# Optimization experiments

Measured on AMD Instinct MI355X. Metric: run time of the kernel, lower is better.

## Reference

```python
import jax, jax.numpy as jnp
import numpy as np

N = 16384      # nodes (radar cells x batched graphs)
H = 128        # n_hidden
N_ENV = 7
N_IN = N_ENV + 2 + 1  # env + coords + density = 10
T_CTX = 24
HORIZON = 40
T = T_CTX + HORIZON


def setup_inputs() -> dict:
    key = jax.random.key(0)
    ks = jax.random.split(key, 40)

    def w(k, shape, fan_in):
        return jax.random.normal(k, shape, jnp.float32) * np.float32(1.0 / np.sqrt(fan_in))

    inp = {}
    inp["x"] = jax.random.normal(ks[0], (N, T), jnp.float32)
    inp["coords"] = jax.random.normal(ks[1], (N, 2), jnp.float32)
    inp["env"] = jax.random.normal(ks[2], (N, N_ENV, T), jnp.float32)
    # --- encoder params ---
    inp["enc_W_in"] = w(ks[3], (H, N_IN), N_IN)           # Linear(n_in->H), no bias
    inp["enc_Wih0"] = w(ks[4], (4 * H, H), H)
    inp["enc_Whh0"] = w(ks[5], (4 * H, H), H)
    inp["enc_bih0"] = jnp.zeros((4 * H,), jnp.float32)
    inp["enc_bhh0"] = jnp.zeros((4 * H,), jnp.float32)
    inp["enc_Wih1"] = w(ks[6], (4 * H, H), H)
    inp["enc_Whh1"] = w(ks[7], (4 * H, H), H)
    inp["enc_bih1"] = jnp.zeros((4 * H,), jnp.float32)
    inp["enc_bhh1"] = jnp.zeros((4 * H,), jnp.float32)
    # --- NodeLSTM params ---
    inp["node_W_in"] = w(ks[8], (H, N_IN), N_IN)          # Linear(n_in->H), no bias
    inp["in_Wih"] = w(ks[9], (4 * H, 2 * H), 2 * H)       # lstm_in takes [inputs, enc_state]
    inp["in_Whh"] = w(ks[10], (4 * H, H), H)
    inp["in_bih"] = jnp.zeros((4 * H,), jnp.float32)
    inp["in_bhh"] = jnp.zeros((4 * H,), jnp.float32)
    inp["l1_Wih"] = w(ks[11], (4 * H, H), H)
    inp["l1_Whh"] = w(ks[12], (4 * H, H), H)
    inp["l1_bih"] = jnp.zeros((4 * H,), jnp.float32)
    inp["l1_bhh"] = jnp.zeros((4 * H,), jnp.float32)
    # hidden2in / hidden2out heads: Linear(H,H) -> ReLU -> Linear(H,1)
    inp["h2in_W1"] = w(ks[13], (H, H), H)
    inp["h2in_b1"] = jnp.zeros((H,), jnp.float32)
    inp["h2in_W2"] = w(ks[14], (1, H), H)
    inp["h2in_b2"] = jnp.zeros((1,), jnp.float32)
    inp["h2out_W1"] = w(ks[15], (H, H), H)
    inp["h2out_b1"] = jnp.zeros((H,), jnp.float32)
    inp["h2out_W2"] = w(ks[16], (1, H), H)
    inp["h2out_b2"] = jnp.zeros((1,), jnp.float32)
    return inp


def _lstm_cell(xin, h, c, Wih, Whh, bih, bhh):
    # torch.nn.LSTMCell semantics; gate order i, f, g, o
    gates = xin @ Wih.T + h @ Whh.T + (bih + bhh)
    i, f, g, o = jnp.split(gates, 4, axis=1)
    c_new = jax.nn.sigmoid(f) * c + jax.nn.sigmoid(i) * jnp.tanh(g)
    h_new = jax.nn.sigmoid(o) * jnp.tanh(c_new)
    return h_new, c_new


def reference(x, coords, env,
              enc_W_in, enc_Wih0, enc_Whh0, enc_bih0, enc_bhh0,
              enc_Wih1, enc_Whh1, enc_bih1, enc_bhh1,
              node_W_in, in_Wih, in_Whh, in_bih, in_bhh,
              l1_Wih, l1_Whh, l1_bih, l1_bhh,
              h2in_W1, h2in_b1, h2in_W2, h2in_b2,
              h2out_W1, h2out_b1, h2out_W2, h2out_b2):
    n = x.shape[0]
    z = jnp.zeros((n, H), x.dtype)

    # ---------- encoder: scan over T_CTX context steps ----------
    def enc_step(carry, xs):
        h0, c0, h1, c1 = carry
        xt, et = xs  # [N], [N, N_ENV]
        inp = jnp.concatenate([xt[:, None], coords, et], axis=1) @ enc_W_in.T
        h0, c0 = _lstm_cell(inp, h0, c0, enc_Wih0, enc_Whh0, enc_bih0, enc_bhh0)
        h1, c1 = _lstm_cell(h0, h1, c1, enc_Wih1, enc_Whh1, enc_bih1, enc_bhh1)
        return (h0, c0, h1, c1), None

    enc_xs = (x[:, :T_CTX].T, jnp.moveaxis(env[:, :, :T_CTX], 2, 0))
    (h0, c0, h1, c1), _ = jax.lax.scan(enc_step, (z, z, z, z), enc_xs)
    enc_state = h1  # h[-1] captured at setup_states, fixed over the horizon

    def head(hid, W1, b1, W2, b2):
        return jax.nn.sigmoid(jax.nn.relu(hid @ W1.T + b1) @ W2.T + b2)

    # ---------- decoder: scan over HORIZON forecast steps ----------
    def dec_step(carry, et):
        xc, h0, c0, h1, c1 = carry
        inp = jnp.concatenate([xc, coords, et], axis=1) @ node_W_in.T
        inp = jnp.concatenate([inp, enc_state], axis=1)  # [N, 2H]
        h0, c0 = _lstm_cell(inp, h0, c0, in_Wih, in_Whh, in_bih, in_bhh)
        h1, c1 = _lstm_cell(h0, h1, c1, l1_Wih, l1_Whh, l1_bih, l1_bhh)
        x_in = head(h1, h2in_W1, h2in_b1, h2in_W2, h2in_b2)
        x_out = head(h1, h2out_W1, h2out_b1, h2out_W2, h2out_b2)
        xn = xc + x_in - x_out * xc  # source/sink update, [N, 1]
        return (xn, h0, c0, h1, c1), xn

    x0 = x[:, T_CTX - 1][:, None]
    dec_xs = jnp.moveaxis(env[:, :, T_CTX:T_CTX + HORIZON], 2, 0)
    _, ys = jax.lax.scan(dec_step, (x0, h0, c0, h1, c1), dec_xs)  # [HORIZON, N, 1]
    return jnp.transpose(ys[..., 0], (1, 0))  # [N, HORIZON]
```

## Files before the change

kernel.cpp:

```cpp
#include <hip/hip_runtime.h>
#include <hip/hip_bf16.h>
#include <cstdint>
#include <cstddef>

typedef __bf16 bf16_t;
typedef bf16_t bf16x8 __attribute__((ext_vector_type(8)));
typedef bf16_t bf16x4 __attribute__((ext_vector_type(4)));
typedef float  f32x4  __attribute__((ext_vector_type(4)));

#define TT    64
#define T_CTX 24
#define HOR   40
#define SA    264
#define NTH   512

#define MFMA __builtin_amdgcn_mfma_f32_16x16x32_bf16

#define O_PKE   16
#define O_PKD   (O_PKE + 262144)
#define O_PKX   (O_PKD + 294912)
#define O_BIAS  (O_PKX + 131072)
#define O_HEADP (O_BIAS + 2048)
#define O_WINE  (O_HEADP + 512)
#define O_WINN  (O_WINE + 1536)
#define O_B2    (O_WINN + 1536)

struct Ptrs { const void* q[29]; };

__device__ __forceinline__ float sigm(float x) {
  return __builtin_amdgcn_rcpf(1.f + __expf(-x));
}
__device__ __forceinline__ float tanh_(float x) {
  return 1.f - 2.f * __builtin_amdgcn_rcpf(1.f + __expf(2.f * x));
}
__device__ __forceinline__ unsigned pk2(float a, float b) {
  unsigned ua = __float_as_uint(a), ub = __float_as_uint(b);
  ua = (ua + 0x7fffu + ((ua >> 16) & 1u)) >> 16;
  ub = (ub + 0x7fffu + ((ub >> 16) & 1u)) >> 16;
  return ua | (ub << 16);
}
__device__ __forceinline__ float uplo(unsigned p){ return __uint_as_float(p << 16); }
__device__ __forceinline__ float uphi(unsigned p){ return __uint_as_float(p & 0xffff0000u); }

__global__ void detect_kernel(const unsigned short* __restrict__ wsrc, int* __restrict__ flag)
{
  int tid = threadIdx.x;
  int wild = 0;
  for (int i = tid; i < 256; i += 64) {
    unsigned short b = wsrc[i];
    float v  = __uint_as_float(((unsigned)b) << 16);
    float av = fabsf(v);
    unsigned e = (b >> 7) & 0xff;
    if (av > 1000.f || e == 0xff || (((b & 0x7fff) != 0) && av < 1e-9f)) wild++;
  }
  for (int off = 32; off; off >>= 1) wild += __shfl_down(wild, off, 64);
  if (tid == 0) flag[0] = (wild > 16) ? 1 : 0;
}

__global__ void prep_kernel(Ptrs P, bf16_t* __restrict__ wb, const int* __restrict__ flag)
{
  const bool f32 = (flag[0] != 0);
  const int gtid = blockIdx.x * blockDim.x + threadIdx.x;
  const int gsz  = gridDim.x * blockDim.x;
  auto rd = [&](const void* src, int i) -> float {
    return f32 ? ((const float*)src)[i] : (float)((const bf16_t*)src)[i];
  };

  for (int i = gtid; i < 262144; i += gsz) {
    int w = i >> 15, r = i & 32767, f = r >> 9, e = r & 511;
    int ln = e >> 3, j = e & 7;
    int seg = f >> 5, fk = f & 31, kt = fk >> 2, g = fk & 3;
    int row = g * 128 + w * 16 + (ln & 15);
    int col = kt * 32 + ((ln >> 4) << 3) + j;
    float v;
    if (seg == 0) v = (col < 128) ? rd(P.q[4], row * 128 + col) : rd(P.q[5], row * 128 + col - 128);
    else          v = (col < 128) ? rd(P.q[8], row * 128 + col) : rd(P.q[9], row * 128 + col - 128);
    wb[O_PKE + i] = (bf16_t)v;
  }
  for (int i = gtid; i < 294912; i += gsz) {
    int w = i / 36864, r = i - w * 36864, f = r >> 9, e = r & 511;
    int ln = e >> 3, j = e & 7;
    int colk = ((ln >> 4) << 3) + j;
    float v;
    if (f < 64) {
      int seg = f >> 5, fk = f & 31, kt = fk >> 2, g = fk & 3;
      int row = g * 128 + w * 16 + (ln & 15);
      int col = kt * 32 + colk;
      if (seg == 0) v = (col < 128) ? rd(P.q[13], row * 256 + col) : rd(P.q[14], row * 128 + col - 128);
      else          v = (col < 128) ? rd(P.q[17], row * 128 + col) : rd(P.q[18], row * 128 + col - 128);
    } else {
      int f2 = f - 64, h = f2 >> 2, kt = f2 & 3;
      int row = w * 16 + (ln & 15);
      int col = kt * 32 + colk;
      v = rd(h ? P.q[25] : P.q[21], row * 128 + col);
    }
    wb[O_PKD + i] = (bf16_t)v;
  }
  for (int i = gtid; i < 131072; i += gsz) {
    int w = i >> 14, r = i & 16383, f = r >> 9, e = r & 511;
    int ln = e >> 3, j = e & 7;
    int kt = f >> 2, g = f & 3;
    int row = g * 128 + w * 16 + (ln & 15);
    int col = kt * 32 + ((ln >> 4) << 3) + j;
    wb[O_PKX + i] = (bf16_t)rd(P.q[13], row * 256 + 128 + col);
  }
  for (int i = gtid; i < 512; i += gsz) {
    wb[O_BIAS + i]        = (bf16_t)(rd(P.q[6],  i) + rd(P.q[7],  i));
    wb[O_BIAS + 512 + i]  = (bf16_t)(rd(P.q[10], i) + rd(P.q[11], i));
    wb[O_BIAS + 1024 + i] = (bf16_t)(rd(P.q[15], i) + rd(P.q[16], i));
    wb[O_BIAS + 1536 + i] = (bf16_t)(rd(P.q[19], i) + rd(P.q[20], i));
  }
  for (int i = gtid; i < 128; i += gsz) {
    wb[O_HEADP + i]       = (bf16_t)rd(P.q[22], i);
    wb[O_HEADP + 128 + i] = (bf16_t)rd(P.q[23], i);
    wb[O_HEADP + 256 + i] = (bf16_t)rd(P.q[26], i);
    wb[O_HEADP + 384 + i] = (bf16_t)rd(P.q[27], i);
  }
  for (int i = gtid; i < 1536; i += gsz) {
    int cc = i / 12, j = i % 12;
    wb[O_WINE + i] = (j < 10) ? (bf16_t)rd(P.q[3],  cc * 10 + j) : (bf16_t)0.f;
    wb[O_WINN + i] = (j < 10) ? (bf16_t)rd(P.q[12], cc * 10 + j) : (bf16_t)0.f;
  }
  if (gtid == 0) {
    wb[O_B2]     = (bf16_t)rd(P.q[24], 0);
    wb[O_B2 + 1] = (bf16_t)rd(P.q[28], 0);
  }
}

struct PreB { bf16x8 b[2][4]; };

__device__ __forceinline__ PreB preB(const bf16_t* __restrict__ pl) {
  PreB r;
#pragma unroll
  for (int p = 0; p < 2; ++p)
#pragma unroll
    for (int g = 0; g < 4; ++g)
      r.b[p][g] = *(const bf16x8*)(pl + (p * 4 + g) * 512);
  return r;
}

template<int NKT>
__device__ __forceinline__ void gemm_pk(f32x4 (&acc)[4][4], const bf16_t* __restrict__ As,
                                        const bf16_t* __restrict__ pl, const PreB& pre,
                                        int l, int q)
{
  bf16x8 bw[3][4];
#pragma unroll
  for (int g = 0; g < 4; ++g) { bw[0][g] = pre.b[0][g]; bw[1][g] = pre.b[1][g]; }
#pragma unroll
  for (int kt = 0; kt < NKT; ++kt) {
    bf16x8 a[4];
#pragma unroll
    for (int mt = 0; mt < 4; ++mt)
      a[mt] = *(const bf16x8*)(As + (mt * 16 + l) * SA + kt * 32 + q * 8);
    if (kt + 2 < NKT) {
#pragma unroll
      for (int g = 0; g < 4; ++g)
        bw[(kt + 2) % 3][g] = *(const bf16x8*)(pl + ((kt + 2) * 4 + g) * 512);
    }
#pragma unroll
    for (int g = 0; g < 4; ++g) {
      bf16x8 b = bw[kt % 3][g];
      acc[g][0] = MFMA(a[0], b, acc[g][0], 0, 0, 0);
      acc[g][1] = MFMA(a[1], b, acc[g][1], 0, 0, 0);
      acc[g][2] = MFMA(a[2], b, acc[g][2], 0, 0, 0);
      acc[g][3] = MFMA(a[3], b, acc[g][3], 0, 0, 0);
    }
  }
}

template<bool DUAL>
__device__ __forceinline__ void cell_up(f32x4 (&acc)[4][4], float (&c)[16],
                                        bf16_t* __restrict__ shb, bf16_t* __restrict__ sha,
                                        const bf16_t* __restrict__ bias,
                                        int wid, int l, int q)
{
  const int jc = wid * 16 + l;
  const float bi  = (float)bias[jc];
  const float bf_ = (float)bias[128 + jc];
  const float bg  = (float)bias[256 + jc];
  const float bo  = (float)bias[384 + jc];
#pragma unroll
  for (int mt = 0; mt < 4; ++mt) {
#pragma unroll
    for (int r = 0; r < 4; ++r) {
      float gi = acc[0][mt][r] + bi;
      float gf = acc[1][mt][r] + bf_;
      float gg = acc[2][mt][r] + bg;
      float go = acc[3][mt][r] + bo;
      float cn = sigm(gf) * c[mt * 4 + r] + sigm(gi) * tanh_(gg);
      float hh = sigm(go) * tanh_(cn);
      c[mt * 4 + r] = cn;
      const int row = mt * 16 + q * 4 + r;
      shb[row * SA + jc] = (bf16_t)hh;
      if (DUAL) sha[row * SA + jc] = (bf16_t)hh;
    }
  }
}

__device__ __forceinline__ void proj16(const float* v, const bf16_t* __restrict__ wbase,
                                       bf16_t* __restrict__ sx, int nd, int sub)
{
  bf16x8 o0, o1;
#pragma unroll
  for (int cc = 0; cc < 16; ++cc) {
    const bf16_t* wr = wbase + (sub * 16 + cc) * 12;
    bf16x4 w0 = *(const bf16x4*)(wr);
    bf16x4 w1 = *(const bf16x4*)(wr + 4);
    bf16x4 w2 = *(const bf16x4*)(wr + 8);
    float a = v[0] * (float)w0[0] + v[1] * (float)w0[1] + v[2] * (float)w0[2] + v[3] * (float)w0[3]
            + v[4] * (float)w1[0] + v[5] * (float)w1[1] + v[6] * (float)w1[2] + v[7] * (float)w1[3]
            + v[8] * (float)w2[0] + v[9] * (float)w2[1];
    if (cc < 8) o0[cc] = (bf16_t)a; else o1[cc - 8] = (bf16_t)a;
  }
  *(bf16x8*)(sx + nd * SA + sub * 16)     = o0;
  *(bf16x8*)(sx + nd * SA + sub * 16 + 8) = o1;
}

template<typename T>
__global__ __launch_bounds__(NTH, 2) void lstm_persist(
    const T* __restrict__ x, const T* __restrict__ coords, const T* __restrict__ env,
    const bf16_t* __restrict__ w, const int* __restrict__ flag, T* __restrict__ out)
{
  const bool want_f32 = (sizeof(T) == 4);
  if ((flag[0] != 0) != want_f32) return;

  __shared__ __align__(16) bf16_t bufA[64 * SA];
  __shared__ __align__(16) bf16_t bufB[64 * SA];
  __shared__ __align__(16) bf16_t s_win[2 * 128 * 12];
  __shared__ __align__(16) bf16_t s_bias[4 * 512];
  __shared__ float s_red[128];
  __shared__ float s_xc[64];

  const int tid  = threadIdx.x;
  const int wid  = tid >> 6;
  const int lane = tid & 63;
  const int l    = tid & 15;
  const int q    = (tid & 63) >> 4;
  const int node0 = blockIdx.x * 64;
  const int nd  = tid >> 3;
  const int sub = tid & 7;

  const bf16_t* plE0 = w + O_PKE + wid * 32768 + lane * 8;
  const bf16_t* plE1 = plE0 + 16384;
  const bf16_t* plD0 = w + O_PKD + wid * 36864 + lane * 8;
  const bf16_t* plD1 = plD0 + 16384;
  const bf16_t* plH  = plD0 + 32768;
  const bf16_t* plX  = w + O_PKX + wid * 16384 + lane * 8;

  for (int i = tid; i < 2048; i += NTH) s_bias[i] = w[O_BIAS + i];
  for (int i = tid; i < 3072; i += NTH) s_win[i]  = w[O_WINE + i];
  for (int i = tid; i < 64 * SA; i += NTH) { bufA[i] = (bf16_t)0.f; bufB[i] = (bf16_t)0.f; }

  const float cx = (float)coords[(size_t)(node0 + nd) * 2 + 0];
  const float cy = (float)coords[(size_t)(node0 + nd) * 2 + 1];

  float c0[16], c1[16];
#pragma unroll
  for (int i = 0; i < 16; ++i) { c0[i] = 0.f; c1[i] = 0.f; }

  PreB pA = preB(plE0);
  __syncthreads();

#pragma unroll 1
  for (int t = 0; t < T_CTX; ++t) {
    float v[10];
    v[0] = (float)x[(size_t)(node0 + nd) * TT + t];
    v[1] = cx; v[2] = cy;
#pragma unroll
    for (int e = 0; e < 7; ++e)
      v[3 + e] = (float)env[((size_t)(node0 + nd) * 7 + e) * TT + t];
    proj16(v, s_win, bufA, nd, sub);
    __syncthreads();

    f32x4 acc[4][4];
#pragma unroll
    for (int g = 0; g < 4; ++g)
#pragma unroll
      for (int mt = 0; mt < 4; ++mt) acc[g][mt] = f32x4{0.f, 0.f, 0.f, 0.f};
    gemm_pk<8>(acc, bufA, plE0, pA, l, q);
    PreB pC = preB(plE1);
    __syncthreads();
    cell_up<true>(acc, c0, bufB, bufA + 128, s_bias, wid, l, q);
    __syncthreads();

#pragma unroll
    for (int g = 0; g < 4; ++g)
#pragma unroll
      for (int mt = 0; mt < 4; ++mt) acc[g][mt] = f32x4{0.f, 0.f, 0.f, 0.f};
    gemm_pk<8>(acc, bufB, plE1, pC, l, q);
    pA = preB((t < T_CTX - 1) ? plE0 : plX);
    __syncthreads();
    cell_up<false>(acc, c1, bufB + 128, nullptr, s_bias + 512, wid, l, q);
  }
  __syncthreads();

  uint2 geh[4][4];
  {
    f32x4 acc[4][4];
#pragma unroll
    for (int g = 0; g < 4; ++g)
#pragma unroll
      for (int mt = 0; mt < 4; ++mt) acc[g][mt] = f32x4{0.f, 0.f, 0.f, 0.f};
    gemm_pk<4>(acc, bufB + 128, plX, pA, l, q);
#pragma unroll
    for (int g = 0; g < 4; ++g)
#pragma unroll
      for (int mt = 0; mt < 4; ++mt)
        geh[g][mt] = uint2{pk2(acc[g][mt][0], acc[g][mt][1]),
                           pk2(acc[g][mt][2], acc[g][mt][3])};
  }
  if (tid < 64) s_xc[tid] = (float)x[(size_t)(node0 + tid) * TT + (T_CTX - 1)];
  const float b2i = (float)w[O_B2];
  const float b2o = (float)w[O_B2 + 1];
  const float b1i = (float)w[O_HEADP + wid * 16 + l];
  const float w2i = (float)w[O_HEADP + 128 + wid * 16 + l];
  const float b1o = (float)w[O_HEADP + 256 + wid * 16 + l];
  const float w2o = (float)w[O_HEADP + 384 + wid * 16 + l];
  pA = preB(plD0);
  __syncthreads();

#pragma unroll 1
  for (int s = 0; s < HOR; ++s) {
    const int t = T_CTX + s;
    float v[10];
    v[0] = s_xc[nd];
    v[1] = cx; v[2] = cy;
#pragma unroll
    for (int e = 0; e < 7; ++e)
      v[3 + e] = (float)env[((size_t)(node0 + nd) * 7 + e) * TT + t];
    proj16(v, s_win + 1536, bufA, nd, sub);
    __syncthreads();

    f32x4 acc[4][4];
#pragma unroll
    for (int g = 0; g < 4; ++g)
#pragma unroll
      for (int mt = 0; mt < 4; ++mt)
        acc[g][mt] = f32x4{uplo(geh[g][mt].x), uphi(geh[g][mt].x),
                           uplo(geh[g][mt].y), uphi(geh[g][mt].y)};
    gemm_pk<8>(acc, bufA, plD0, pA, l, q);
    PreB pC = preB(plD1);
    __syncthreads();
    cell_up<true>(acc, c0, bufB, bufA + 128, s_bias + 1024, wid, l, q);
    __syncthreads();

#pragma unroll
    for (int g = 0; g < 4; ++g)
#pragma unroll
      for (int mt = 0; mt < 4; ++mt) acc[g][mt] = f32x4{0.f, 0.f, 0.f, 0.f};
    gemm_pk<8>(acc, bufB, plD1, pC, l, q);
    bf16x8 hb[8];
#pragma unroll
    for (int f = 0; f < 8; ++f) hb[f] = *(const bf16x8*)(plH + f * 512);
    __syncthreads();
    cell_up<false>(acc, c1, bufB + 128, nullptr, s_bias + 1536, wid, l, q);
    if (tid < 128) s_red[tid] = 0.f;
    pA = preB(plD0);
    __syncthreads();

    f32x4 hacc[2][4];
#pragma unroll
    for (int hd = 0; hd < 2; ++hd)
#pragma unroll
      for (int mt = 0; mt < 4; ++mt) hacc[hd][mt] = f32x4{0.f, 0.f, 0.f, 0.f};
#pragma unroll
    for (int kt = 0; kt < 4; ++kt) {
      bf16x8 a[4];
#pragma unroll
      for (int mt = 0; mt < 4; ++mt)
        a[mt] = *(const bf16x8*)(bufB + 128 + (mt * 16 + l) * SA + kt * 32 + q * 8);
#pragma unroll
      for (int mt = 0; mt < 4; ++mt) {
        hacc[0][mt] = MFMA(a[mt], hb[kt],     hacc[0][mt], 0, 0, 0);
        hacc[1][mt] = MFMA(a[mt], hb[4 + kt], hacc[1][mt], 0, 0, 0);
      }
    }
#pragma unroll
    for (int hd = 0; hd < 2; ++hd) {
      const float b1v = hd ? b1o : b1i;
      const float w2v = hd ? w2o : w2i;
#pragma unroll
      for (int mt = 0; mt < 4; ++mt)
#pragma unroll
        for (int r = 0; r < 4; ++r) {
          float val = fmaxf(hacc[hd][mt][r] + b1v, 0.f) * w2v;
          val += __shfl_xor(val, 1, 64);
          val += __shfl_xor(val, 2, 64);
          val += __shfl_xor(val, 4, 64);
          val += __shfl_xor(val, 8, 64);
          if (l == 0) atomicAdd(&s_red[hd * 64 + mt * 16 + q * 4 + r], val);
        }
    }
    __syncthreads();
    if (tid < 64) {
      float xc = s_xc[tid];
      float si = sigm(s_red[tid] + b2i);
      float so = sigm(s_red[64 + tid] + b2o);
      float xn = xc + si - so * xc;
      s_xc[tid] = xn;
      out[(size_t)(node0 + tid) * HOR + s] = (T)xn;
    }
    __syncthreads();
  }
}

extern "C" void kernel_launch(void* const* d_in, const int* in_sizes, int n_in,
                              void* d_out, int out_size, void* d_ws, size_t ws_size,
                              hipStream_t stream) {
  (void)in_sizes; (void)n_in; (void)out_size; (void)ws_size;
  Ptrs P;
  for (int i = 0; i < 29; ++i) P.q[i] = d_in[i];
  int*    flag = (int*)d_ws;
  bf16_t* w    = (bf16_t*)d_ws;

  detect_kernel<<<1, 64, 0, stream>>>((const unsigned short*)d_in[4], flag);
  prep_kernel<<<256, 256, 0, stream>>>(P, w, flag);
  lstm_persist<float><<<256, NTH, 0, stream>>>(
      (const float*)d_in[0], (const float*)d_in[1], (const float*)d_in[2],
      w, flag, (float*)d_out);
  lstm_persist<bf16_t><<<256, NTH, 0, stream>>>(
      (const bf16_t*)d_in[0], (const bf16_t*)d_in[1], (const bf16_t*)d_in[2],
      w, flag, (bf16_t*)d_out);
}
```

Before: 2.159 ms.

## Stage env in LDS, deepen B prefetch, buffer outputs, relocate packed weights

```diff
diff --git a/kernel.cpp b/kernel.cpp
--- a/kernel.cpp
+++ b/kernel.cpp
@@ -16,14 +16,15 @@
 
 #define MFMA __builtin_amdgcn_mfma_f32_16x16x32_bf16
 
-#define O_PKE   16
-#define O_PKD   (O_PKE + 262144)
-#define O_PKX   (O_PKD + 294912)
+#define DO_PKD  262144
+
+#define O_PKX   16
 #define O_BIAS  (O_PKX + 131072)
 #define O_HEADP (O_BIAS + 2048)
 #define O_WINE  (O_HEADP + 512)
 #define O_WINN  (O_WINE + 1536)
 #define O_B2    (O_WINN + 1536)
+#define O_OUTS  (O_B2 + 16)
 
 struct Ptrs { const void* q[29]; };
 
@@ -57,7 +58,8 @@
   if (tid == 0) flag[0] = (wild > 16) ? 1 : 0;
 }
 
-__global__ void prep_kernel(Ptrs P, bf16_t* __restrict__ wb, const int* __restrict__ flag)
+__global__ void prep_kernel(Ptrs P, bf16_t* __restrict__ wb, bf16_t* __restrict__ so,
+                            const int* __restrict__ flag)
 {
   const bool f32 = (flag[0] != 0);
   const int gtid = blockIdx.x * blockDim.x + threadIdx.x;
@@ -75,7 +77,7 @@
     float v;
     if (seg == 0) v = (col < 128) ? rd(P.q[4], row * 128 + col) : rd(P.q[5], row * 128 + col - 128);
     else          v = (col < 128) ? rd(P.q[8], row * 128 + col) : rd(P.q[9], row * 128 + col - 128);
-    wb[O_PKE + i] = (bf16_t)v;
+    so[i] = (bf16_t)v;
   }
   for (int i = gtid; i < 294912; i += gsz) {
     int w = i / 36864, r = i - w * 36864, f = r >> 9, e = r & 511;
@@ -94,7 +96,7 @@
       int col = kt * 32 + colk;
       v = rd(h ? P.q[25] : P.q[21], row * 128 + col);
     }
-    wb[O_PKD + i] = (bf16_t)v;
+    so[DO_PKD + i] = (bf16_t)v;
   }
   for (int i = gtid; i < 131072; i += gsz) {
     int w = i >> 14, r = i & 16383, f = r >> 9, e = r & 511;
@@ -127,12 +129,12 @@
   }
 }
 
-struct PreB { bf16x8 b[2][4]; };
+struct PreB { bf16x8 b[3][4]; };
 
 __device__ __forceinline__ PreB preB(const bf16_t* __restrict__ pl) {
   PreB r;
 #pragma unroll
-  for (int p = 0; p < 2; ++p)
+  for (int p = 0; p < 3; ++p)
 #pragma unroll
     for (int g = 0; g < 4; ++g)
       r.b[p][g] = *(const bf16x8*)(pl + (p * 4 + g) * 512);
@@ -141,30 +143,32 @@
 
 template<int NKT>
 __device__ __forceinline__ void gemm_pk(f32x4 (&acc)[4][4], const bf16_t* __restrict__ As,
-                                        const bf16_t* __restrict__ pl, const PreB& pre,
+                                        const bf16_t* __restrict__ pl, PreB pre,
                                         int l, int q)
 {
-  bf16x8 bw[3][4];
-#pragma unroll
-  for (int g = 0; g < 4; ++g) { bw[0][g] = pre.b[0][g]; bw[1][g] = pre.b[1][g]; }
 #pragma unroll
   for (int kt = 0; kt < NKT; ++kt) {
     bf16x8 a[4];
 #pragma unroll
     for (int mt = 0; mt < 4; ++mt)
       a[mt] = *(const bf16x8*)(As + (mt * 16 + l) * SA + kt * 32 + q * 8);
-    if (kt + 2 < NKT) {
+    bf16x8 nb[4];
+    if (kt + 3 < NKT) {
 #pragma unroll
       for (int g = 0; g < 4; ++g)
-        bw[(kt + 2) % 3][g] = *(const bf16x8*)(pl + ((kt + 2) * 4 + g) * 512);
+        nb[g] = *(const bf16x8*)(pl + ((kt + 3) * 4 + g) * 512);
     }
 #pragma unroll
     for (int g = 0; g < 4; ++g) {
-      bf16x8 b = bw[kt % 3][g];
+      bf16x8 b = pre.b[kt % 3][g];
       acc[g][0] = MFMA(a[0], b, acc[g][0], 0, 0, 0);
       acc[g][1] = MFMA(a[1], b, acc[g][1], 0, 0, 0);
       acc[g][2] = MFMA(a[2], b, acc[g][2], 0, 0, 0);
       acc[g][3] = MFMA(a[3], b, acc[g][3], 0, 0, 0);
+    }
+    if (kt + 3 < NKT) {
+#pragma unroll
+      for (int g = 0; g < 4; ++g) pre.b[kt % 3][g] = nb[g];
     }
   }
 }
@@ -220,7 +224,8 @@
 template<typename T>
 __global__ __launch_bounds__(NTH, 2) void lstm_persist(
     const T* __restrict__ x, const T* __restrict__ coords, const T* __restrict__ env,
-    const bf16_t* __restrict__ w, const int* __restrict__ flag, T* __restrict__ out)
+    const bf16_t* __restrict__ w, const bf16_t* __restrict__ sw,
+    const int* __restrict__ flag, float* __restrict__ wsout)
 {
   const bool want_f32 = (sizeof(T) == 4);
   if ((flag[0] != 0) != want_f32) return;
@@ -231,6 +236,8 @@
   __shared__ __align__(16) bf16_t s_bias[4 * 512];
   __shared__ float s_red[128];
   __shared__ float s_xc[64];
+  __shared__ float s_env[2][64][8];
+  __shared__ float s_out[64 * 40];
 
   const int tid  = threadIdx.x;
   const int wid  = tid >> 6;
@@ -240,10 +247,12 @@
   const int node0 = blockIdx.x * 64;
   const int nd  = tid >> 3;
   const int sub = tid & 7;
-
-  const bf16_t* plE0 = w + O_PKE + wid * 32768 + lane * 8;
+  const int nd_e = tid / 7;
+  const int e_e  = tid - nd_e * 7;
+
+  const bf16_t* plE0 = sw + wid * 32768 + lane * 8;
   const bf16_t* plE1 = plE0 + 16384;
-  const bf16_t* plD0 = w + O_PKD + wid * 36864 + lane * 8;
+  const bf16_t* plD0 = sw + DO_PKD + wid * 36864 + lane * 8;
   const bf16_t* plD1 = plD0 + 16384;
   const bf16_t* plH  = plD0 + 32768;
   const bf16_t* plX  = w + O_PKX + wid * 16384 + lane * 8;
@@ -252,6 +261,9 @@
   for (int i = tid; i < 3072; i += NTH) s_win[i]  = w[O_WINE + i];
   for (int i = tid; i < 64 * SA; i += NTH) { bufA[i] = (bf16_t)0.f; bufB[i] = (bf16_t)0.f; }
 
+  if (tid < 448) s_env[0][nd_e][e_e] = (float)env[(size_t)((node0 + nd_e) * 7 + e_e) * TT];
+  else           s_env[0][tid - 448][7] = (float)x[(size_t)(node0 + tid - 448) * TT];
+
   const float cx = (float)coords[(size_t)(node0 + nd) * 2 + 0];
   const float cy = (float)coords[(size_t)(node0 + nd) * 2 + 1];
 
@@ -264,13 +276,20 @@
 
 #pragma unroll 1
   for (int t = 0; t < T_CTX; ++t) {
+    const int tn = t + 1;
+    float tpre = 0.f;
+    if (tid < 448) tpre = (float)env[(size_t)((node0 + nd_e) * 7 + e_e) * TT + tn];
+    else           tpre = (float)x[(size_t)(node0 + tid - 448) * TT + tn];
+
     float v[10];
-    v[0] = (float)x[(size_t)(node0 + nd) * TT + t];
+    v[0] = s_env[t & 1][nd][7];
     v[1] = cx; v[2] = cy;
 #pragma unroll
-    for (int e = 0; e < 7; ++e)
-      v[3 + e] = (float)env[((size_t)(node0 + nd) * 7 + e) * TT + t];
+    for (int e = 0; e < 7; ++e) v[3 + e] = s_env[t & 1][nd][e];
     proj16(v, s_win, bufA, nd, sub);
+
+    if (tid < 448) s_env[tn & 1][nd_e][e_e] = tpre;
+    else           s_env[tn & 1][tid - 448][7] = tpre;
     __syncthreads();
 
     f32x4 acc[4][4];
@@ -317,19 +336,30 @@
   const float w2i = (float)w[O_HEADP + 128 + wid * 16 + l];
   const float b1o = (float)w[O_HEADP + 256 + wid * 16 + l];
   const float w2o = (float)w[O_HEADP + 384 + wid * 16 + l];
-  pA = preB(plD0);
+  PreB pD = preB(plD0);
   __syncthreads();
 
 #pragma unroll 1
   for (int s = 0; s < HOR; ++s) {
     const int t = T_CTX + s;
+    const int tn = t + 1;
+    float tpre = 0.f;
+    if (tn < TT) {
+      if (tid < 448) tpre = (float)env[(size_t)((node0 + nd_e) * 7 + e_e) * TT + tn];
+      else           tpre = (float)x[(size_t)(node0 + tid - 448) * TT + tn];
+    }
+
     float v[10];
     v[0] = s_xc[nd];
     v[1] = cx; v[2] = cy;
 #pragma unroll
-    for (int e = 0; e < 7; ++e)
-      v[3 + e] = (float)env[((size_t)(node0 + nd) * 7 + e) * TT + t];
+    for (int e = 0; e < 7; ++e) v[3 + e] = s_env[t & 1][nd][e];
     proj16(v, s_win + 1536, bufA, nd, sub);
+
+    if (tn < TT) {
+      if (tid < 448) s_env[tn & 1][nd_e][e_e] = tpre;
+      else           s_env[tn & 1][tid - 448][7] = tpre;
+    }
     __syncthreads();
 
     f32x4 acc[4][4];
@@ -339,7 +369,7 @@
       for (int mt = 0; mt < 4; ++mt)
         acc[g][mt] = f32x4{uplo(geh[g][mt].x), uphi(geh[g][mt].x),
                            uplo(geh[g][mt].y), uphi(geh[g][mt].y)};
-    gemm_pk<8>(acc, bufA, plD0, pA, l, q);
+    gemm_pk<8>(acc, bufA, plD0, pD, l, q);
     PreB pC = preB(plD1);
     __syncthreads();
     cell_up<true>(acc, c0, bufB, bufA + 128, s_bias + 1024, wid, l, q);
@@ -356,7 +386,7 @@
     __syncthreads();
     cell_up<false>(acc, c1, bufB + 128, nullptr, s_bias + 1536, wid, l, q);
     if (tid < 128) s_red[tid] = 0.f;
-    pA = preB(plD0);
+    pD = preB(plD0);
     __syncthreads();
 
     f32x4 hacc[2][4];
@@ -399,10 +429,23 @@
       float so = sigm(s_red[64 + tid] + b2o);
       float xn = xc + si - so * xc;
       s_xc[tid] = xn;
-      out[(size_t)(node0 + tid) * HOR + s] = (T)xn;
-    }
-    __syncthreads();
-  }
+      s_out[tid * 40 + s] = xn;
+    }
+    __syncthreads();
+  }
+
+  for (int i = tid; i < 64 * 40; i += NTH)
+    wsout[(size_t)node0 * 40 + i] = s_out[i];
+}
+
+template<typename T>
+__global__ void out_copy(const float* __restrict__ wsout, const int* __restrict__ flag,
+                         T* __restrict__ out)
+{
+  const bool want_f32 = (sizeof(T) == 4);
+  if ((flag[0] != 0) != want_f32) return;
+  int i = blockIdx.x * blockDim.x + threadIdx.x;
+  if (i < 16384 * HOR) out[i] = (T)wsout[i];
 }
 
 extern "C" void kernel_launch(void* const* d_in, const int* in_sizes, int n_in,
@@ -413,13 +456,17 @@
   for (int i = 0; i < 29; ++i) P.q[i] = d_in[i];
   int*    flag = (int*)d_ws;
   bf16_t* w    = (bf16_t*)d_ws;
+  bf16_t* so   = (bf16_t*)d_out;
+  float*  wsout = (float*)(w + O_OUTS);
 
   detect_kernel<<<1, 64, 0, stream>>>((const unsigned short*)d_in[4], flag);
-  prep_kernel<<<256, 256, 0, stream>>>(P, w, flag);
+  prep_kernel<<<256, 256, 0, stream>>>(P, w, so, flag);
   lstm_persist<float><<<256, NTH, 0, stream>>>(
       (const float*)d_in[0], (const float*)d_in[1], (const float*)d_in[2],
-      w, flag, (float*)d_out);
+      w, so, flag, wsout);
   lstm_persist<bf16_t><<<256, NTH, 0, stream>>>(
       (const bf16_t*)d_in[0], (const bf16_t*)d_in[1], (const bf16_t*)d_in[2],
-      w, flag, (bf16_t*)d_out);
-}
+      w, so, flag, wsout);
+  out_copy<float><<<2560, 256, 0, stream>>>(wsout, flag, (float*)d_out);
+  out_copy<bf16_t><<<2560, 256, 0, stream>>>(wsout, flag, (bf16_t*)d_out);
+}
```

New measurement: 2.595 ms. 1.2x slower.
